# Optimization experiments

Measured on AMD Instinct MI355X. Metric: run time of the kernel, lower is better.

## Reference

```python
import jax, jax.numpy as jnp
import numpy as np

B, T, D_IN, D_PROJ, D_OUT, MEM = 8, 2048, 1024, 1024, 1024, 40


def setup_inputs() -> dict:
    key = jax.random.key(0)
    k1, k2, k3, k4 = jax.random.split(key, 4)
    x = jax.random.normal(k1, (B, T, D_IN), dtype=jnp.float32)
    # xavier-uniform-style params
    lim1 = np.sqrt(6.0 / (D_IN + D_PROJ))
    lim2 = np.sqrt(6.0 / (D_PROJ + D_OUT))
    limm = np.sqrt(6.0 / (MEM + 1 + D_PROJ))
    W1 = jax.random.uniform(k2, (D_IN, D_PROJ), minval=-lim1, maxval=lim1, dtype=jnp.float32)
    W2 = jax.random.uniform(k3, (D_PROJ, D_OUT), minval=-lim2, maxval=lim2, dtype=jnp.float32)
    mw = jax.random.uniform(k4, (MEM + 1, D_PROJ), minval=-limm, maxval=limm, dtype=jnp.float32)
    mw = mw.at[0].set(0.0)  # row 0 zeroed at init (still trainable in the original)
    bias1 = jnp.ones((D_PROJ,), dtype=jnp.float32)
    bias2 = jnp.ones((D_OUT,), dtype=jnp.float32)
    return {"input_data": x, "W1": W1, "bias1": bias1, "W2": W2, "bias2": bias2,
            "memory_weights": mw}


def _fsmn_memory(p, memory_weights):
    # p: [B, T, D], memory_weights: [M+1, D]
    # Original gather index: mm[i,j] = i-j+1 for 0<=i-j<=M-1, else 0.
    # => out[b,i,d] = sum_{l=0}^{M-1} w[l+1,d]*p[b,i-l,d]
    #              + w[0,d] * (sum_j p[b,j,d] - sum_{l=0}^{M-1} p[b,i-l,d])
    M = memory_weights.shape[0] - 1
    b, t, d = p.shape
    # causal depthwise conv: taps w[1:] with lag l -> kernel position M-1-l
    rhs = memory_weights[1:][::-1].T[:, None, :]           # [D, 1, M]
    lhs = jnp.pad(p.transpose(0, 2, 1), ((0, 0), (0, 0), (M - 1, 0)))  # [B, D, T+M-1]
    band = jax.lax.conv_general_dilated(
        lhs, rhs, window_strides=(1,), padding='VALID',
        feature_group_count=d,
        dimension_numbers=('NCH', 'OIH', 'NCH')).transpose(0, 2, 1)    # [B, T, D]
    # in-band running sum via cumsum difference
    cs = jnp.cumsum(p, axis=1)                              # [B, T, D]
    band_sum = cs - jnp.pad(cs, ((0, 0), (M, 0), (0, 0)))[:, :t]
    total = cs[:, -1:]                                      # [B, 1, D]
    return band + memory_weights[0] * (total - band_sum)


def reference(input_data, W1, bias1, W2, bias2, memory_weights):
    p = jnp.matmul(input_data, W1) + bias1                  # [B, T, D_PROJ]
    p = _fsmn_memory(p, memory_weights)
    return jnp.matmul(p, W2) + bias2                        # [B, T, D_OUT]
```

## Files before the change

kernel.cpp:

```cpp
#include <hip/hip_runtime.h>

typedef __attribute__((ext_vector_type(8))) short bf16x8;
typedef __attribute__((ext_vector_type(4))) float f32x4;
typedef __attribute__((ext_vector_type(8))) unsigned short u16x8;

typedef const __attribute__((address_space(1))) void* as1cv;
typedef __attribute__((address_space(3))) void* as3v;

__device__ __forceinline__ unsigned short f2bf(float f) {
    union { float f; unsigned u; } x; x.f = f;
    unsigned r = x.u + 0x7FFFu + ((x.u >> 16) & 1u);
    return (unsigned short)(r >> 16);
}
__device__ __forceinline__ float bf2f(unsigned short u) {
    union { unsigned u; float f; } x; x.u = ((unsigned)u) << 16; return x.f;
}

__global__ __launch_bounds__(256) void k_prep(
    const float* __restrict__ x, unsigned short* __restrict__ x_bf, long n,
    const float* __restrict__ W1, unsigned short* __restrict__ W1t,
    const float* __restrict__ W2, unsigned short* __restrict__ W2t,
    float* __restrict__ totals)
{
    __shared__ float tile[64][65];
    const int bid = blockIdx.x;
    const int tid = threadIdx.x;
    if (bid < 512) {
        const float* W = (bid >= 256) ? W2 : W1;
        unsigned short* Wt = (bid >= 256) ? W2t : W1t;
        const int rem = bid & 255;
        const int r0 = (rem >> 4) * 64, c0 = (rem & 15) * 64;
        #pragma unroll
        for (int i = 0; i < 16; ++i) {
            int idx = tid + i * 256;
            int r = idx >> 6, c = idx & 63;
            tile[r][c] = W[(long)(r0 + r) * 1024 + (c0 + c)];
        }
        __syncthreads();
        #pragma unroll
        for (int i = 0; i < 16; ++i) {
            int idx = tid + i * 256;
            int r = idx >> 6, c = idx & 63;
            Wt[(long)(c0 + r) * 1024 + (r0 + c)] = f2bf(tile[c][r]);
        }
    } else if (bid < 2560) {
        long i = (long)(bid - 512) * 256 + tid;
        const long stride = 2048L * 256;
        const long n4 = n >> 2;
        for (long j = i; j < n4; j += stride) {
            float4 v = ((const float4*)x)[j];
            ushort4 o;
            o.x = f2bf(v.x); o.y = f2bf(v.y); o.z = f2bf(v.z); o.w = f2bf(v.w);
            ((ushort4*)x_bf)[j] = o;
        }
    } else {
        #pragma unroll
        for (int i = 0; i < 32; ++i)
            totals[tid + i * 256] = 0.f;
    }
}

template<int OUT_BF16, int DO_COLSUM>
__global__ __launch_bounds__(512, 2) void k_gemm256(
    const unsigned short* __restrict__ A,
    const unsigned short* __restrict__ Bt,
    const float* __restrict__ bias,
    void* __restrict__ C,
    float* __restrict__ totals,
    int M, int N, int K)
{
    __shared__ unsigned short lds[2][4][8192];
    const int tid  = threadIdx.x;
    const int lane = tid & 63;
    const int w    = tid >> 6;
    const int wm   = w >> 2;
    const int wn   = w & 3;

    const int nwg = gridDim.x;
    const int cpx = nwg >> 3;
    const int wg  = (blockIdx.x & 7) * cpx + (blockIdx.x >> 3);
    const int nblks = N >> 8;
    const int mblk = wg / nblks, nblk = wg % nblks;
    const long m0 = (long)mblk << 8, n0 = (long)nblk << 8;

    const int segRow  = lane >> 3;
    const long segColE = (long)(((lane & 7) ^ segRow) << 3);

    const int rr = lane & 15, cc = lane >> 4;
    const int smask = (rr & 7) << 4;
    const int colSwz0 = (((cc * 16) ^ smask) >> 1);
    const int colSwz1 = (((64 + cc * 16) ^ smask) >> 1);

    auto stage = [&](int buf, int slot, const unsigned short* src, long rowBase, int kt) {
        #pragma unroll
        for (int g = 0; g < 2; ++g) {
            const int s = w + g * 8;
            const unsigned short* gp = src + (rowBase + s * 8 + segRow) * (long)K
                                           + (long)kt * 64 + segColE;
            __builtin_amdgcn_global_load_lds((as1cv)gp,
                (as3v)(&lds[buf][slot][s * 512 + lane * 8]), 16, 0, 0);
        }
    };

    f32x4 acc[8][4];
    #pragma unroll
    for (int i = 0; i < 8; ++i)
        #pragma unroll
        for (int j = 0; j < 4; ++j)
            acc[i][j] = (f32x4){0.f, 0.f, 0.f, 0.f};

    bf16x8 bfrag[4][2];
    const int bRowBase = (wn & 1) * 64;
    const int NK = K >> 6;
    const int ITERS = K >> 7;

#define VM4   asm volatile("s_waitcnt vmcnt(4)" ::: "memory")
#define BAR   __builtin_amdgcn_s_barrier()
#define PH(BUF, Q, STAGES, VMW) do {                                                 \
    bf16x8 af0_0, af0_1, af1_0, af1_1;                                               \
    { const unsigned short* Ah = &lds[BUF][wm][0];                                   \
      af0_0 = *(const bf16x8*)(Ah + ((Q)*32 + rr) * 64 + colSwz0);                   \
      af0_1 = *(const bf16x8*)(Ah + ((Q)*32 + rr) * 64 + colSwz1);                   \
      af1_0 = *(const bf16x8*)(Ah + ((Q)*32 + 16 + rr) * 64 + colSwz0);              \
      af1_1 = *(const bf16x8*)(Ah + ((Q)*32 + 16 + rr) * 64 + colSwz1); }            \
    if ((Q) == 0) { const unsigned short* Bh = &lds[BUF][2 + (wn >> 1)][0];          \
      _Pragma("unroll")                                                              \
      for (int nj = 0; nj < 4; ++nj) {                                               \
        bfrag[nj][0] = *(const bf16x8*)(Bh + (bRowBase + nj*16 + rr) * 64 + colSwz0);\
        bfrag[nj][1] = *(const bf16x8*)(Bh + (bRowBase + nj*16 + rr) * 64 + colSwz1);\
      } }                                                                            \
    STAGES;                                                                          \
    VMW;                                                                             \
    asm volatile("s_waitcnt lgkmcnt(0)" ::: "memory");                               \
    __builtin_amdgcn_sched_barrier(0);                                               \
    __builtin_amdgcn_s_setprio(1);                                                   \
    _Pragma("unroll")                                                                \
    for (int nj = 0; nj < 4; ++nj) {                                                 \
      acc[2*(Q)][nj]   = __builtin_amdgcn_mfma_f32_16x16x32_bf16(af0_0, bfrag[nj][0], acc[2*(Q)][nj],   0,0,0); \
      acc[2*(Q)][nj]   = __builtin_amdgcn_mfma_f32_16x16x32_bf16(af0_1, bfrag[nj][1], acc[2*(Q)][nj],   0,0,0); \
      acc[2*(Q)+1][nj] = __builtin_amdgcn_mfma_f32_16x16x32_bf16(af1_0, bfrag[nj][0], acc[2*(Q)+1][nj], 0,0,0); \
      acc[2*(Q)+1][nj] = __builtin_amdgcn_mfma_f32_16x16x32_bf16(af1_1, bfrag[nj][1], acc[2*(Q)+1][nj], 0,0,0); \
    }                                                                                \
    __builtin_amdgcn_s_setprio(0);                                                   \
} while (0)

    stage(0, 0, A,  m0,       0);
    stage(0, 1, A,  m0 + 128, 0);
    stage(0, 2, Bt, n0,       0);
    stage(0, 3, Bt, n0 + 128, 0);
    stage(1, 2, Bt, n0,       1);
    stage(1, 3, Bt, n0 + 128, 1);
    VM4;
    BAR;

    for (int it = 0; it < ITERS; ++it) {
        const int kt1 = 2 * it + 1;
        int kt2 = 2 * it + 2; if (kt2 >= NK) kt2 = 0;
        int kt3 = 2 * it + 3; if (kt3 >= NK) kt3 = 1;

        PH(0, 0, stage(1, 0, A,  m0,       kt1), );
        PH(0, 1, stage(1, 1, A,  m0 + 128, kt1), );
        BAR;
        PH(0, 2, { stage(0, 2, Bt, n0, kt2); stage(0, 3, Bt, n0 + 128, kt2); }, );
        PH(0, 3, , VM4);
        BAR;
        PH(1, 0, stage(0, 0, A,  m0,       kt2), );
        PH(1, 1, stage(0, 1, A,  m0 + 128, kt2), );
        BAR;
        PH(1, 2, { stage(1, 2, Bt, n0, kt3); stage(1, 3, Bt, n0 + 128, kt3); }, );
        PH(1, 3, , VM4);
        BAR;
    }
#undef PH
#undef BAR
#undef VM4

    float cs[4] = {0.f, 0.f, 0.f, 0.f};
    #pragma unroll
    for (int mi = 0; mi < 8; ++mi) {
        const long rowb = m0 + wm * 128 + mi * 16 + cc * 4;
        #pragma unroll
        for (int nj = 0; nj < 4; ++nj) {
            const long col = n0 + wn * 64 + nj * 16 + rr;
            const float bv = bias[col];
            #pragma unroll
            for (int jj = 0; jj < 4; ++jj) {
                const float v = acc[mi][nj][jj] + bv;
                if (DO_COLSUM) cs[nj] += v;
                if (OUT_BF16) ((unsigned short*)C)[(rowb + jj) * N + col] = f2bf(v);
                else          ((float*)C)[(rowb + jj) * N + col] = v;
            }
        }
    }
    if (DO_COLSUM) {
        const int b = (int)(m0 >> 11);
        #pragma unroll
        for (int nj = 0; nj < 4; ++nj) {
            float c0 = cs[nj];
            c0 += __shfl_xor(c0, 16, 64);
            c0 += __shfl_xor(c0, 32, 64);
            if (cc == 0)
                atomicAdd(totals + b * 1024 + n0 + wn * 64 + nj * 16 + rr, c0);
        }
    }
}

#define FS_ROWS 167
__global__ __launch_bounds__(256, 2) void k_fsmn(
    const unsigned short* __restrict__ p,
    const float* __restrict__ mw,
    const float* __restrict__ total,
    unsigned short* __restrict__ p2,
    int T)
{
    __shared__ unsigned short sp[FS_ROWS][64];
    __shared__ float smw[41][64];
    const int b  = blockIdx.z;
    const int t0 = blockIdx.y * 128;
    const int d0 = blockIdx.x * 64;
    const int tid = threadIdx.x;

    for (int idx = tid; idx < 41 * 64; idx += 256) {
        int r = idx >> 6, c = idx & 63;
        smw[r][c] = mw[r * 1024 + d0 + c];
    }
    {
        const int row0 = tid >> 3;
        const int col8 = (tid & 7) * 8;
        #pragma unroll
        for (int i = 0; i < 6; ++i) {
            const int row = row0 + i * 32;
            if (row < FS_ROWS) {
                const int t = t0 + row - 39;
                u16x8 v = {0, 0, 0, 0, 0, 0, 0, 0};
                if (t >= 0)
                    v = *(const u16x8*)(p + ((long)b * T + t) * 1024 + d0 + col8);
                *(u16x8*)(&sp[row][col8]) = v;
            }
        }
    }
    __syncthreads();

    const int lane = tid & 63, wv = tid >> 6;
    const int d = d0 + lane;

    float m[40];
    #pragma unroll
    for (int l = 0; l < 40; ++l) m[l] = smw[l + 1][lane];
    const float m0v = smw[0][lane];
    const float tot = total[b * 1024 + d];

    #pragma unroll
    for (int pass = 0; pass < 2; ++pass) {
        const int obase = wv * 32 + pass * 16;
        float w[55];
        #pragma unroll
        for (int j = 0; j < 55; ++j) w[j] = bf2f(sp[obase + j][lane]);

        float acc[16];
        #pragma unroll
        for (int s = 0; s < 16; ++s) acc[s] = 0.f;
        #pragma unroll
        for (int lag = 0; lag < 40; ++lag) {
            const float mm = m[lag];
            #pragma unroll
            for (int s = 0; s < 16; ++s)
                acc[s] = fmaf(mm, w[s + 39 - lag], acc[s]);
        }

        float accw[16];
        {
            float S = 0.f;
            #pragma unroll
            for (int j = 0; j < 40; ++j) S += w[j];
            accw[0] = S;
            #pragma unroll
            for (int s = 1; s < 16; ++s) accw[s] = accw[s - 1] + w[s + 39] - w[s - 1];
        }

        unsigned short* ob = p2 + ((long)b * T + t0 + obase) * 1024 + d;
        #pragma unroll
        for (int s = 0; s < 16; ++s)
            ob[(long)s * 1024] = f2bf(acc[s] + m0v * (tot - accw[s]));
    }
}

extern "C" void kernel_launch(void* const* d_in, const int* in_sizes, int n_in,
                              void* d_out, int out_size, void* d_ws, size_t ws_size,
                              hipStream_t stream) {
    const float* x  = (const float*)d_in[0];
    const float* W1 = (const float*)d_in[1];
    const float* b1 = (const float*)d_in[2];
    const float* W2 = (const float*)d_in[3];
    const float* b2 = (const float*)d_in[4];
    const float* mw = (const float*)d_in[5];
    float* out = (float*)d_out;

    const int B = 8, T = 2048;
    const long M = (long)B * T;
    const int N = 1024, K = 1024;

    char* ws = (char*)d_ws;
    unsigned short* x_bf   = (unsigned short*)(ws);
    unsigned short* W1t    = (unsigned short*)(ws + 33554432L);
    unsigned short* W2t    = (unsigned short*)(ws + 35651584L);
    unsigned short* p_bf   = (unsigned short*)(ws + 37748736L);
    float*          totals = (float*)(ws + 71303168L);
    unsigned short* p2_bf  = x_bf;

    k_prep<<<2561, 256, 0, stream>>>(x, x_bf, M * 1024, W1, W1t, W2, W2t, totals);

    k_gemm256<1, 1><<<dim3((int)((M / 256) * (N / 256))), 512, 0, stream>>>(
        x_bf, W1t, b1, (void*)p_bf, totals, (int)M, N, K);

    k_fsmn<<<dim3(1024 / 64, T / 128, B), 256, 0, stream>>>(p_bf, mw, totals, p2_bf, T);

    k_gemm256<0, 0><<<dim3((int)((M / 256) * (N / 256))), 512, 0, stream>>>(
        p2_bf, W2t, b2, (void*)out, nullptr, (int)M, N, K);
}
```

Before: 124.3 us.

## Fuse prep, both GEMMs and FSMN into one cooperative persistent kernel

```diff
diff --git a/kernel.cpp b/kernel.cpp
--- a/kernel.cpp
+++ b/kernel.cpp
@@ -1,4 +1,5 @@
 #include <hip/hip_runtime.h>
+#include <hip/hip_cooperative_groups.h>
 
 typedef __attribute__((ext_vector_type(8))) short bf16x8;
 typedef __attribute__((ext_vector_type(4))) float f32x4;
@@ -16,61 +17,16 @@
     union { unsigned u; float f; } x; x.u = ((unsigned)u) << 16; return x.f;
 }
 
-__global__ __launch_bounds__(256) void k_prep(
-    const float* __restrict__ x, unsigned short* __restrict__ x_bf, long n,
-    const float* __restrict__ W1, unsigned short* __restrict__ W1t,
-    const float* __restrict__ W2, unsigned short* __restrict__ W2t,
-    float* __restrict__ totals)
-{
-    __shared__ float tile[64][65];
-    const int bid = blockIdx.x;
-    const int tid = threadIdx.x;
-    if (bid < 512) {
-        const float* W = (bid >= 256) ? W2 : W1;
-        unsigned short* Wt = (bid >= 256) ? W2t : W1t;
-        const int rem = bid & 255;
-        const int r0 = (rem >> 4) * 64, c0 = (rem & 15) * 64;
-        #pragma unroll
-        for (int i = 0; i < 16; ++i) {
-            int idx = tid + i * 256;
-            int r = idx >> 6, c = idx & 63;
-            tile[r][c] = W[(long)(r0 + r) * 1024 + (c0 + c)];
-        }
-        __syncthreads();
-        #pragma unroll
-        for (int i = 0; i < 16; ++i) {
-            int idx = tid + i * 256;
-            int r = idx >> 6, c = idx & 63;
-            Wt[(long)(c0 + r) * 1024 + (r0 + c)] = f2bf(tile[c][r]);
-        }
-    } else if (bid < 2560) {
-        long i = (long)(bid - 512) * 256 + tid;
-        const long stride = 2048L * 256;
-        const long n4 = n >> 2;
-        for (long j = i; j < n4; j += stride) {
-            float4 v = ((const float4*)x)[j];
-            ushort4 o;
-            o.x = f2bf(v.x); o.y = f2bf(v.y); o.z = f2bf(v.z); o.w = f2bf(v.w);
-            ((ushort4*)x_bf)[j] = o;
-        }
-    } else {
-        #pragma unroll
-        for (int i = 0; i < 32; ++i)
-            totals[tid + i * 256] = 0.f;
-    }
-}
-
 template<int OUT_BF16, int DO_COLSUM>
-__global__ __launch_bounds__(512, 2) void k_gemm256(
+__device__ __forceinline__ void gemm_body(
+    unsigned short (*lds)[4][8192],
     const unsigned short* __restrict__ A,
     const unsigned short* __restrict__ Bt,
     const float* __restrict__ bias,
     void* __restrict__ C,
     float* __restrict__ totals,
-    int M, int N, int K)
+    int M, int N, int K, int bid, int tid)
 {
-    __shared__ unsigned short lds[2][4][8192];
-    const int tid  = threadIdx.x;
     const int lane = tid & 63;
     const int w    = tid >> 6;
     const int wm   = w >> 2;
@@ -78,7 +34,7 @@
 
     const int nwg = gridDim.x;
     const int cpx = nwg >> 3;
-    const int wg  = (blockIdx.x & 7) * cpx + (blockIdx.x >> 3);
+    const int wg  = (bid & 7) * cpx + (bid >> 3);
     const int nblks = N >> 8;
     const int mblk = wg / nblks, nblk = wg % nblks;
     const long m0 = (long)mblk << 8, n0 = (long)nblk << 8;
@@ -206,83 +162,139 @@
 }
 
 #define FS_ROWS 167
-__global__ __launch_bounds__(256, 2) void k_fsmn(
-    const unsigned short* __restrict__ p,
+__global__ __launch_bounds__(512, 2) void k_fused(
+    const float* __restrict__ x,
+    const float* __restrict__ W1, const float* __restrict__ b1,
+    const float* __restrict__ W2, const float* __restrict__ b2,
     const float* __restrict__ mw,
-    const float* __restrict__ total,
-    unsigned short* __restrict__ p2,
-    int T)
+    float* __restrict__ out,
+    char* __restrict__ ws)
 {
-    __shared__ unsigned short sp[FS_ROWS][64];
-    __shared__ float smw[41][64];
-    const int b  = blockIdx.z;
-    const int t0 = blockIdx.y * 128;
-    const int d0 = blockIdx.x * 64;
+    __shared__ unsigned short lds[2][4][8192];
+    char* smem = (char*)(&lds[0][0][0]);
+
+    unsigned short* x_bf   = (unsigned short*)(ws);
+    unsigned short* W1t    = (unsigned short*)(ws + 33554432L);
+    unsigned short* W2t    = (unsigned short*)(ws + 35651584L);
+    unsigned short* p_bf   = (unsigned short*)(ws + 37748736L);
+    float*          totals = (float*)(ws + 71303168L);
+    unsigned short* p2_bf  = x_bf;
+
+    const int bid = blockIdx.x;
     const int tid = threadIdx.x;
-
-    for (int idx = tid; idx < 41 * 64; idx += 256) {
-        int r = idx >> 6, c = idx & 63;
-        smw[r][c] = mw[r * 1024 + d0 + c];
-    }
+    const int B = 8, T = 2048;
+    const long M = (long)B * T;
+    const int N = 1024, K = 1024;
+
+    cooperative_groups::grid_group grid = cooperative_groups::this_grid();
+
     {
+        float (*tile)[65] = (float (*)[65])smem;
+        #pragma unroll
+        for (int wsel = 0; wsel < 2; ++wsel) {
+            const float* W = wsel ? W2 : W1;
+            unsigned short* Wt = wsel ? W2t : W1t;
+            const int r0 = (bid >> 4) * 64, c0 = (bid & 15) * 64;
+            #pragma unroll
+            for (int i = 0; i < 8; ++i) {
+                int idx = tid + i * 512;
+                int r = idx >> 6, c = idx & 63;
+                tile[r][c] = W[(long)(r0 + r) * 1024 + (c0 + c)];
+            }
+            __syncthreads();
+            #pragma unroll
+            for (int i = 0; i < 8; ++i) {
+                int idx = tid + i * 512;
+                int r = idx >> 6, c = idx & 63;
+                Wt[(long)(c0 + r) * 1024 + (r0 + c)] = f2bf(tile[c][r]);
+            }
+            __syncthreads();
+        }
+        if (bid == 0) {
+            #pragma unroll
+            for (int i = 0; i < 16; ++i) totals[tid + i * 512] = 0.f;
+        }
+        const long n4 = (M * 1024) >> 2;
+        for (long j = (long)bid * 512 + tid; j < n4; j += 131072) {
+            float4 v = ((const float4*)x)[j];
+            ushort4 o;
+            o.x = f2bf(v.x); o.y = f2bf(v.y); o.z = f2bf(v.z); o.w = f2bf(v.w);
+            ((ushort4*)x_bf)[j] = o;
+        }
+    }
+    grid.sync();
+
+    gemm_body<1, 1>(lds, x_bf, W1t, b1, (void*)p_bf, totals, (int)M, N, K, bid, tid);
+    grid.sync();
+
+    {
+        unsigned short (*sp)[64] = (unsigned short (*)[64])smem;
+        float (*smw)[64] = (float (*)[64])(smem + 21504);
+        const int d0 = (bid >> 4) * 64;
+        for (int idx = tid; idx < 41 * 64; idx += 512) {
+            int r = idx >> 6, c = idx & 63;
+            smw[r][c] = mw[r * 1024 + d0 + c];
+        }
+        __syncthreads();
+        const int lane = tid & 63, wv = tid >> 6;
+        float m[40];
+        #pragma unroll
+        for (int l = 0; l < 40; ++l) m[l] = smw[l + 1][lane];
+        const float m0v = smw[0][lane];
+
         const int row0 = tid >> 3;
         const int col8 = (tid & 7) * 8;
-        #pragma unroll
-        for (int i = 0; i < 6; ++i) {
-            const int row = row0 + i * 32;
-            if (row < FS_ROWS) {
-                const int t = t0 + row - 39;
-                u16x8 v = {0, 0, 0, 0, 0, 0, 0, 0};
-                if (t >= 0)
-                    v = *(const u16x8*)(p + ((long)b * T + t) * 1024 + d0 + col8);
-                *(u16x8*)(&sp[row][col8]) = v;
-            }
-        }
-    }
-    __syncthreads();
-
-    const int lane = tid & 63, wv = tid >> 6;
-    const int d = d0 + lane;
-
-    float m[40];
-    #pragma unroll
-    for (int l = 0; l < 40; ++l) m[l] = smw[l + 1][lane];
-    const float m0v = smw[0][lane];
-    const float tot = total[b * 1024 + d];
-
-    #pragma unroll
-    for (int pass = 0; pass < 2; ++pass) {
-        const int obase = wv * 32 + pass * 16;
-        float w[55];
-        #pragma unroll
-        for (int j = 0; j < 55; ++j) w[j] = bf2f(sp[obase + j][lane]);
-
-        float acc[16];
-        #pragma unroll
-        for (int s = 0; s < 16; ++s) acc[s] = 0.f;
-        #pragma unroll
-        for (int lag = 0; lag < 40; ++lag) {
-            const float mm = m[lag];
+        for (int u = 0; u < 8; ++u) {
+            const int j = (bid & 15) * 8 + u;
+            const int b = j >> 4, tchunk = j & 15;
+            const int t0 = tchunk * 128;
+            __syncthreads();
+            #pragma unroll
+            for (int i = 0; i < 3; ++i) {
+                const int row = row0 + i * 64;
+                if (row < FS_ROWS) {
+                    const int t = t0 + row - 39;
+                    u16x8 v = {0, 0, 0, 0, 0, 0, 0, 0};
+                    if (t >= 0)
+                        v = *(const u16x8*)(p_bf + ((long)b * T + t) * 1024 + d0 + col8);
+                    *(u16x8*)(&sp[row][col8]) = v;
+                }
+            }
+            __syncthreads();
+
+            const float tot = totals[b * 1024 + d0 + lane];
+            float w[55];
+            #pragma unroll
+            for (int j2 = 0; j2 < 55; ++j2) w[j2] = bf2f(sp[wv * 16 + j2][lane]);
+
+            float acc[16];
+            #pragma unroll
+            for (int s = 0; s < 16; ++s) acc[s] = 0.f;
+            #pragma unroll
+            for (int lag = 0; lag < 40; ++lag) {
+                const float mm = m[lag];
+                #pragma unroll
+                for (int s = 0; s < 16; ++s)
+                    acc[s] = fmaf(mm, w[s + 39 - lag], acc[s]);
+            }
+            float accw[16];
+            {
+                float S = 0.f;
+                #pragma unroll
+                for (int j2 = 0; j2 < 40; ++j2) S += w[j2];
+                accw[0] = S;
+                #pragma unroll
+                for (int s = 1; s < 16; ++s) accw[s] = accw[s - 1] + w[s + 39] - w[s - 1];
+            }
+            unsigned short* ob = p2_bf + ((long)b * T + t0 + wv * 16) * 1024 + d0 + lane;
             #pragma unroll
             for (int s = 0; s < 16; ++s)
-                acc[s] = fmaf(mm, w[s + 39 - lag], acc[s]);
-        }
-
-        float accw[16];
-        {
-            float S = 0.f;
-            #pragma unroll
-            for (int j = 0; j < 40; ++j) S += w[j];
-            accw[0] = S;
-            #pragma unroll
-            for (int s = 1; s < 16; ++s) accw[s] = accw[s - 1] + w[s + 39] - w[s - 1];
-        }
-
-        unsigned short* ob = p2 + ((long)b * T + t0 + obase) * 1024 + d;
-        #pragma unroll
-        for (int s = 0; s < 16; ++s)
-            ob[(long)s * 1024] = f2bf(acc[s] + m0v * (tot - accw[s]));
-    }
+                ob[(long)s * 1024] = f2bf(acc[s] + m0v * (tot - accw[s]));
+        }
+    }
+    grid.sync();
+
+    gemm_body<0, 0>(lds, p2_bf, W2t, b2, (void*)out, nullptr, (int)M, N, K, bid, tid);
 }
 
 extern "C" void kernel_launch(void* const* d_in, const int* in_sizes, int n_in,
@@ -295,26 +307,10 @@
     const float* b2 = (const float*)d_in[4];
     const float* mw = (const float*)d_in[5];
     float* out = (float*)d_out;
-
-    const int B = 8, T = 2048;
-    const long M = (long)B * T;
-    const int N = 1024, K = 1024;
-
     char* ws = (char*)d_ws;
-    unsigned short* x_bf   = (unsigned short*)(ws);
-    unsigned short* W1t    = (unsigned short*)(ws + 33554432L);
-    unsigned short* W2t    = (unsigned short*)(ws + 35651584L);
-    unsigned short* p_bf   = (unsigned short*)(ws + 37748736L);
-    float*          totals = (float*)(ws + 71303168L);
-    unsigned short* p2_bf  = x_bf;
-
-    k_prep<<<2561, 256, 0, stream>>>(x, x_bf, M * 1024, W1, W1t, W2, W2t, totals);
-
-    k_gemm256<1, 1><<<dim3((int)((M / 256) * (N / 256))), 512, 0, stream>>>(
-        x_bf, W1t, b1, (void*)p_bf, totals, (int)M, N, K);
-
-    k_fsmn<<<dim3(1024 / 64, T / 128, B), 256, 0, stream>>>(p_bf, mw, totals, p2_bf, T);
-
-    k_gemm256<0, 0><<<dim3((int)((M / 256) * (N / 256))), 512, 0, stream>>>(
-        p2_bf, W2t, b2, (void*)out, nullptr, (int)M, N, K);
-}
+
+    void* kargs[] = { (void*)&x, (void*)&W1, (void*)&b1, (void*)&W2, (void*)&b2,
+                      (void*)&mw, (void*)&out, (void*)&ws };
+    hipLaunchCooperativeKernel((const void*)k_fused, dim3(256), dim3(512),
+                               kargs, 0, stream);
+}
```

Result: slower. 220.3 us (+77.2%).
